# Performance work log

Hardware: AMD Instinct MI355X
Metric: run time of the kernel (lower is better)

Reference implementation:

```python
import jax, jax.numpy as jnp
import numpy as np
import math

EPS = 1e-06
C_CONST = 2.0 + EPS
CHUNK = 128


def _features(xc, omega, W_poly, quad_nodes):
    # xc: (B,H,t,D) -> poly:(B,H,t,P), prf:(R,B,H,t,M)
    xn = xc / jnp.clip(jnp.linalg.norm(xc, axis=-1, keepdims=True), 1e-12)  # F.normalize
    poly = jnp.einsum('bhtd,hdp->bhtp', xn, W_poly)
    proj = jnp.einsum('bhtd,rhdm->rbhtm', xn, omega)
    s = quad_nodes[:, None, None, None, None]
    sqrt2s = jnp.sqrt(2.0 * jnp.clip(s, 0.0))
    M = omega.shape[-1]
    prf = jnp.exp(jnp.clip(proj * sqrt2s - s, -20.0, 20.0)) / math.sqrt(M)
    return poly, prf


def setup_inputs() -> dict:
    key = jax.random.key(0)
    ks = jax.random.split(key, 6)
    B, T, E, H, D, M, R, P = 1, 1024, 512, 8, 64, 8, 1, 32
    x = jax.random.normal(ks[0], (B, T, E), jnp.float32)
    W_qkv = jax.random.normal(ks[1], (3 * E, E), jnp.float32) / math.sqrt(E)
    b_qkv = jnp.zeros((3 * E,), jnp.float32)
    W_out = jax.random.normal(ks[2], (E, E), jnp.float32) / math.sqrt(E)
    b_out = jnp.zeros((E,), jnp.float32)
    omega = jax.random.normal(ks[3], (R, H, D, M), jnp.float32)
    W_poly = jax.random.normal(ks[4], (H, D, P), jnp.float32) / math.sqrt(D)
    nodes, weights = np.polynomial.laguerre.laggauss(R)
    quad_nodes = jnp.asarray(nodes, jnp.float32) / C_CONST
    quad_weights = jnp.asarray(weights, jnp.float32) / C_CONST
    return {"x": x, "W_qkv": W_qkv, "b_qkv": b_qkv, "W_out": W_out, "b_out": b_out,
            "omega": omega, "W_poly": W_poly, "quad_nodes": quad_nodes, "quad_weights": quad_weights}


def reference(x, W_qkv, b_qkv, W_out, b_out, omega, W_poly, quad_nodes, quad_weights):
    B, T, E = x.shape
    R, H, D, M = omega.shape
    P = W_poly.shape[-1]
    qkv = x @ W_qkv.T + b_qkv
    q, k, v = jnp.split(qkv, 3, axis=-1)

    def to_chunks(a):
        # (B,T,E) -> (Nc,B,H,chunk,D)
        return a.reshape(B, T, H, D).transpose(0, 2, 1, 3).reshape(B, H, T // CHUNK, CHUNK, D).transpose(2, 0, 1, 3, 4)

    qc, kc, vc = map(to_chunks, (q, k, v))
    sqw = jnp.sqrt(jnp.clip(quad_weights, 0.0))[:, None, None, None, None]
    kv0 = jnp.zeros((R, B, H, P, M, D), jnp.float32)
    k0 = jnp.zeros((R, B, H, P, M), jnp.float32)

    def step(carry, inp):
        kv_state, k_state = carry
        qch, kch, vch = inp
        q_poly, q_prf = _features(qch, omega, W_poly, quad_nodes)
        k_poly, k_prf = _features(kch, omega, W_poly, quad_nodes)
        q_prf = q_prf * sqw
        k_prf = k_prf * sqw
        q_outer = jnp.einsum('bhtp,rbhtm->rbhtpm', q_poly, q_prf)
        k_outer = jnp.einsum('bhtp,rbhtm->rbhtpm', k_poly, k_prf)
        kv_prod = jnp.einsum('rbhtpm,bhtd->rbhtpmd', k_outer, vch)
        kv_cur = jnp.cumsum(kv_prod, axis=3) + kv_state[:, :, :, None]
        k_cur = jnp.cumsum(k_outer, axis=3) + k_state[:, :, :, None]
        ctx = jnp.einsum('rbhtpm,rbhtpmd->bhtd', q_outer, kv_cur)  # sums over r too
        den = jnp.einsum('rbhtpm,rbhtpm->bht', q_outer, k_cur)
        out = ctx / jnp.clip(den, 1e-06)[..., None]
        return (kv_cur[:, :, :, -1], k_cur[:, :, :, -1]), out

    _, outs = jax.lax.scan(step, (kv0, k0), (qc, kc, vc))  # (Nc,B,H,chunk,D)
    out = outs.transpose(1, 2, 0, 3, 4).reshape(B, H, T, D).transpose(0, 2, 1, 3).reshape(B, T, E)
    return out @ W_out.T + b_out
```

## Files before the change

kernel.cpp:

```cpp
#include <hip/hip_runtime.h>
#include <math.h>


__global__ __launch_bounds__(256) void gemm_bias_kernel(
    const float* __restrict__ A, const float* __restrict__ W,
    const float* __restrict__ bias, float* __restrict__ C,
    int M, int N, int K)
{
    __shared__ float a_t[16][68];
    __shared__ float w_t[16][68];
    const int tid = threadIdx.x;
    const int n0 = blockIdx.x * 64;
    const int m0 = blockIdx.y * 64;
    const int tx = tid & 15, ty = tid >> 4;
    const int lrow = tid >> 2;
    const int lk4  = (tid & 3) * 4;
    float acc[4][4];
#pragma unroll
    for (int i = 0; i < 4; ++i)
#pragma unroll
        for (int j = 0; j < 4; ++j) acc[i][j] = 0.f;

    for (int k0 = 0; k0 < K; k0 += 16) {
        float4 av = *(const float4*)&A[(m0 + lrow) * K + k0 + lk4];
        float4 wv = *(const float4*)&W[(n0 + lrow) * K + k0 + lk4];
        a_t[lk4 + 0][lrow] = av.x; a_t[lk4 + 1][lrow] = av.y;
        a_t[lk4 + 2][lrow] = av.z; a_t[lk4 + 3][lrow] = av.w;
        w_t[lk4 + 0][lrow] = wv.x; w_t[lk4 + 1][lrow] = wv.y;
        w_t[lk4 + 2][lrow] = wv.z; w_t[lk4 + 3][lrow] = wv.w;
        __syncthreads();
#pragma unroll
        for (int k = 0; k < 16; ++k) {
            float4 af = *(const float4*)&a_t[k][ty * 4];
            float4 wf = *(const float4*)&w_t[k][tx * 4];
            acc[0][0] += af.x * wf.x; acc[0][1] += af.x * wf.y;
            acc[0][2] += af.x * wf.z; acc[0][3] += af.x * wf.w;
            acc[1][0] += af.y * wf.x; acc[1][1] += af.y * wf.y;
            acc[1][2] += af.y * wf.z; acc[1][3] += af.y * wf.w;
            acc[2][0] += af.z * wf.x; acc[2][1] += af.z * wf.y;
            acc[2][2] += af.z * wf.z; acc[2][3] += af.z * wf.w;
            acc[3][0] += af.w * wf.x; acc[3][1] += af.w * wf.y;
            acc[3][2] += af.w * wf.z; acc[3][3] += af.w * wf.w;
        }
        __syncthreads();
    }
    float4 bv = *(const float4*)&bias[n0 + tx * 4];
#pragma unroll
    for (int i = 0; i < 4; ++i) {
        float4 o;
        o.x = acc[i][0] + bv.x; o.y = acc[i][1] + bv.y;
        o.z = acc[i][2] + bv.z; o.w = acc[i][3] + bv.w;
        *(float4*)&C[(m0 + ty * 4 + i) * N + n0 + tx * 4] = o;
    }
}

__global__ __launch_bounds__(256) void features_kernel(
    const float* __restrict__ qkv, const float* __restrict__ omega,
    const float* __restrict__ W_poly, const float* __restrict__ qn,
    const float* __restrict__ qw, float* __restrict__ phi_q,
    float* __restrict__ phi_k)
{
    __shared__ float xn[4][2][64];
    __shared__ float poly[4][2][32];
    __shared__ float prf[4][2][8];
    const int tid = threadIdx.x;
    const int w = tid >> 6;
    const int lane = tid & 63;
    const int item = blockIdx.x * 4 + w;
    const int h = item >> 10;
    const int t = item & 1023;

    float xq = qkv[t * 1536 + h * 64 + lane];
    float xk = qkv[t * 1536 + 512 + h * 64 + lane];
    float sq = xq * xq, sk = xk * xk;
#pragma unroll
    for (int o = 32; o; o >>= 1) { sq += __shfl_xor(sq, o); sk += __shfl_xor(sk, o); }
    float xnq = xq / fmaxf(sqrtf(sq), 1e-12f);
    float xnk = xk / fmaxf(sqrtf(sk), 1e-12f);
    xn[w][0][lane] = xnq;
    xn[w][1][lane] = xnk;
    __syncthreads();

    {
        const int which = lane >> 5;
        const int p = lane & 31;
        float pacc = 0.f;
#pragma unroll 8
        for (int d = 0; d < 64; ++d)
            pacc += xn[w][which][d] * W_poly[(h * 64 + d) * 32 + p];
        poly[w][which][p] = pacc;
    }
    if (lane < 16) {
        const int wh2 = lane >> 3, m = lane & 7;
        float pr = 0.f;
#pragma unroll 8
        for (int d = 0; d < 64; ++d)
            pr += xn[w][wh2][d] * omega[(h * 64 + d) * 8 + m];
        float s0 = qn[0];
        float sqrt2s = sqrtf(2.f * fmaxf(s0, 0.f));
        float sqw = sqrtf(fmaxf(qw[0], 0.f));
        float z = fminf(fmaxf(pr * sqrt2s - s0, -20.f), 20.f);
        prf[w][wh2][m] = expf(z) * 0.3535533905932738f * sqw;
    }
    __syncthreads();

    const int pp = lane >> 1;
    const int mb = (lane & 1) * 4;
    float qp = poly[w][0][pp], kp = poly[w][1][pp];
    float4 oq, ok;
    oq.x = qp * prf[w][0][mb + 0]; oq.y = qp * prf[w][0][mb + 1];
    oq.z = qp * prf[w][0][mb + 2]; oq.w = qp * prf[w][0][mb + 3];
    ok.x = kp * prf[w][1][mb + 0]; ok.y = kp * prf[w][1][mb + 1];
    ok.z = kp * prf[w][1][mb + 2]; ok.w = kp * prf[w][1][mb + 3];
    *(float4*)&phi_q[((h << 10) + t) * 256 + lane * 4] = oq;
    *(float4*)&phi_k[((h << 10) + t) * 256 + lane * 4] = ok;
}

__global__ __launch_bounds__(256) void chunksum_kernel(
    const float* __restrict__ phi_k, const float* __restrict__ qkv,
    float* __restrict__ S_chunk, float* __restrict__ z_chunk)
{
    __shared__ float pk[128][64];
    __shared__ float vv[128][64];
    const int tid = threadIdx.x;
    const int h  = blockIdx.x >> 5;
    const int c  = (blockIdx.x >> 2) & 7;
    const int fg = blockIdx.x & 3;
    const int f0 = fg * 64;

#pragma unroll
    for (int i = 0; i < 8; ++i) {
        int e4 = i * 256 + tid;
        int s = e4 >> 4;
        int f4 = (e4 & 15) * 4;
        *(float4*)&pk[s][f4] =
            *(const float4*)&phi_k[((h << 10) + c * 128 + s) * 256 + f0 + f4];
    }
#pragma unroll
    for (int i = 0; i < 8; ++i) {
        int e4 = i * 256 + tid;
        int s = e4 >> 4;
        int d4 = (e4 & 15) * 4;
        *(float4*)&vv[s][d4] =
            *(const float4*)&qkv[(c * 128 + s) * 1536 + 1024 + h * 64 + d4];
    }
    __syncthreads();

    const int tx = tid & 15;
    const int ty = tid >> 4;
    float acc[4][4];
#pragma unroll
    for (int i = 0; i < 4; ++i)
#pragma unroll
        for (int j = 0; j < 4; ++j) acc[i][j] = 0.f;

    for (int s = 0; s < 128; ++s) {
        float4 pv = *(const float4*)&pk[s][ty * 4];
        float4 v4 = *(const float4*)&vv[s][tx * 4];
        acc[0][0] += pv.x * v4.x; acc[0][1] += pv.x * v4.y;
        acc[0][2] += pv.x * v4.z; acc[0][3] += pv.x * v4.w;
        acc[1][0] += pv.y * v4.x; acc[1][1] += pv.y * v4.y;
        acc[1][2] += pv.y * v4.z; acc[1][3] += pv.y * v4.w;
        acc[2][0] += pv.z * v4.x; acc[2][1] += pv.z * v4.y;
        acc[2][2] += pv.z * v4.z; acc[2][3] += pv.z * v4.w;
        acc[3][0] += pv.w * v4.x; acc[3][1] += pv.w * v4.y;
        acc[3][2] += pv.w * v4.z; acc[3][3] += pv.w * v4.w;
    }

    if (tid < 64) {
        float zacc = 0.f;
        for (int s = 0; s < 128; ++s) zacc += pk[s][tid];
        z_chunk[(h * 8 + c) * 256 + f0 + tid] = zacc;
    }

#pragma unroll
    for (int i = 0; i < 4; ++i) {
        float4 o = make_float4(acc[i][0], acc[i][1], acc[i][2], acc[i][3]);
        *(float4*)&S_chunk[((h * 8 + c) * 256 + f0 + ty * 4 + i) * 64 + tx * 4] = o;
    }
}

__global__ __launch_bounds__(256) void scan_kernel(
    const float* __restrict__ S_chunk, const float* __restrict__ z_chunk,
    float* __restrict__ S_prev, float* __restrict__ z_prev)
{
    int gid = blockIdx.x * 256 + threadIdx.x;
    if (gid < 8 * 256 * 64) {
        int h = gid >> 14;
        int r = gid & 16383;
        float acc = 0.f;
#pragma unroll
        for (int c = 0; c < 8; ++c) {
            int idx = ((h * 8 + c) << 14) + r;
            S_prev[idx] = acc;
            acc += S_chunk[idx];
        }
    }
    if (gid < 2048) {
        int h = gid >> 8, f = gid & 255;
        float acc = 0.f;
#pragma unroll
        for (int c = 0; c < 8; ++c) {
            int idx = (h * 8 + c) * 256 + f;
            z_prev[idx] = acc;
            acc += z_chunk[idx];
        }
    }
}

__global__ __launch_bounds__(256) void attn_kernel(
    const float* __restrict__ phi_q, const float* __restrict__ phi_k,
    const float* __restrict__ qkv, const float* __restrict__ S_prev,
    const float* __restrict__ z_prev, float* __restrict__ attn)
{
    __shared__ float v_lds[128 * 64];
    __shared__ float A_lds[32 * 132];
    __shared__ float phq_t[32][36];
    __shared__ float phk_t[32][132];
    __shared__ float Sst[32][64];
    __shared__ float z_lds[256];
    __shared__ float den_lds[32];
    const int tid = threadIdx.x;
    const int h = blockIdx.x >> 3, c = blockIdx.x & 7;
    const int tb = blockIdx.y * 32;

#pragma unroll
    for (int i = 0; i < 8; ++i) {
        int e4 = i * 256 + tid;
        int s = e4 >> 4;
        int d4 = (e4 & 15) * 4;
        *(float4*)&v_lds[s * 64 + d4] =
            *(const float4*)&qkv[(c * 128 + s) * 1536 + 1024 + h * 64 + d4];
    }
    z_lds[tid] = z_prev[(h * 8 + c) * 256 + tid];

    const int tt = tid >> 5, ss = tid & 31;
    const int d = tid & 63, tg = tid >> 6;
    float acc[4][4];
    float acc2[8];
    float den_acc = 0.f;
#pragma unroll
    for (int i = 0; i < 4; ++i)
#pragma unroll
        for (int j = 0; j < 4; ++j) acc[i][j] = 0.f;
#pragma unroll
    for (int i = 0; i < 8; ++i) acc2[i] = 0.f;

    for (int ft = 0; ft < 8; ++ft) {
        const int f0 = ft * 32;
#pragma unroll
        for (int i = 0; i < 4; ++i) {
            int e = i * 256 + tid;
            int t_ = e >> 5, f = e & 31;
            phq_t[f][t_] = phi_q[((h << 10) + c * 128 + tb + t_) * 256 + f0 + f];
        }
#pragma unroll
        for (int i = 0; i < 16; ++i) {
            int e = i * 256 + tid;
            int s_ = e >> 5, f = e & 31;
            phk_t[f][s_] = phi_k[((h << 10) + c * 128 + s_) * 256 + f0 + f];
        }
#pragma unroll
        for (int i = 0; i < 8; ++i) {
            int e = i * 256 + tid;
            int f = e >> 6, dd = e & 63;
            Sst[f][dd] = S_prev[((h * 8 + c) * 256 + f0 + f) * 64 + dd];
        }
        __syncthreads();
#pragma unroll 4
        for (int f = 0; f < 32; ++f) {
            float4 av = *(const float4*)&phq_t[f][tt * 4];
            float4 bv = *(const float4*)&phk_t[f][ss * 4];
            acc[0][0] += av.x * bv.x; acc[0][1] += av.x * bv.y;
            acc[0][2] += av.x * bv.z; acc[0][3] += av.x * bv.w;
            acc[1][0] += av.y * bv.x; acc[1][1] += av.y * bv.y;
            acc[1][2] += av.y * bv.z; acc[1][3] += av.y * bv.w;
            acc[2][0] += av.z * bv.x; acc[2][1] += av.z * bv.y;
            acc[2][2] += av.z * bv.z; acc[2][3] += av.z * bv.w;
            acc[3][0] += av.w * bv.x; acc[3][1] += av.w * bv.y;
            acc[3][2] += av.w * bv.z; acc[3][3] += av.w * bv.w;
            float sval = Sst[f][d];
            float4 a0 = *(const float4*)&phq_t[f][tg * 8];
            float4 a1 = *(const float4*)&phq_t[f][tg * 8 + 4];
            acc2[0] += a0.x * sval; acc2[1] += a0.y * sval;
            acc2[2] += a0.z * sval; acc2[3] += a0.w * sval;
            acc2[4] += a1.x * sval; acc2[5] += a1.y * sval;
            acc2[6] += a1.z * sval; acc2[7] += a1.w * sval;
        }
        if (tid < 32) {
#pragma unroll
            for (int f = 0; f < 32; ++f)
                den_acc += phq_t[f][tid] * z_lds[f0 + f];
        }
        __syncthreads();
    }
#pragma unroll
    for (int i = 0; i < 4; ++i) {
        float4 o = make_float4(acc[i][0], acc[i][1], acc[i][2], acc[i][3]);
        *(float4*)&A_lds[(tt * 4 + i) * 132 + ss * 4] = o;
    }
    if (tid < 32) den_lds[tid] = den_acc;
    __syncthreads();

#pragma unroll
    for (int i = 0; i < 8; ++i) {
        int tl = tg * 8 + i;
        int tcr = tb + tl;
        float ctx = acc2[i];
        float den = den_lds[tl];
        for (int s = 0; s <= tcr; ++s) {
            float a = A_lds[tl * 132 + s];
            ctx += a * v_lds[s * 64 + d];
            den += a;
        }
        attn[(c * 128 + tcr) * 512 + h * 64 + d] = ctx / fmaxf(den, 1e-6f);
    }
}

extern "C" void kernel_launch(void* const* d_in, const int* in_sizes, int n_in,
                              void* d_out, int out_size, void* d_ws, size_t ws_size,
                              hipStream_t stream)
{
    const float* x      = (const float*)d_in[0];
    const float* W_qkv  = (const float*)d_in[1];
    const float* b_qkv  = (const float*)d_in[2];
    const float* W_out  = (const float*)d_in[3];
    const float* b_out  = (const float*)d_in[4];
    const float* omega  = (const float*)d_in[5];
    const float* W_poly = (const float*)d_in[6];
    const float* qn     = (const float*)d_in[7];
    const float* qw     = (const float*)d_in[8];
    float* out = (float*)d_out;

    float* ws    = (float*)d_ws;
    float* qkv   = ws;
    float* phi_q = qkv + 1572864;
    float* phi_k = phi_q + 2097152;
    float* S_c   = phi_k + 2097152;
    float* z_c   = S_c + 1048576;
    float* S_p   = z_c + 16384;
    float* z_p   = S_p + 1048576;
    float* attn  = z_p + 16384;

    gemm_bias_kernel<<<dim3(24, 16), 256, 0, stream>>>(x, W_qkv, b_qkv, qkv, 1024, 1536, 512);
    features_kernel<<<2048, 256, 0, stream>>>(qkv, omega, W_poly, qn, qw, phi_q, phi_k);
    chunksum_kernel<<<256, 256, 0, stream>>>(phi_k, qkv, S_c, z_c);
    scan_kernel<<<512, 256, 0, stream>>>(S_c, z_c, S_p, z_p);
    attn_kernel<<<dim3(64, 4), 256, 0, stream>>>(phi_q, phi_k, qkv, S_p, z_p, attn);
    gemm_bias_kernel<<<dim3(8, 16), 256, 0, stream>>>(attn, W_out, b_out, out, 1024, 512, 512);
}
```

Before: 198.2 us.

## Split attn kernel into 512-thread warp-specialized halves and skip non-causal key tiles

The attention kernel now launches 512 threads per block. Half compute the intra-chunk q·k scores, the other half compute the inter-chunk q·S context and the denominator, with results passed through a new shared buffer. It also loads only the keys and values up to the causal limit for each query tile and skips score tiles beyond it. The intent is more parallelism per block and less wasted load and FMA work, at the cost of extra shared memory and an extra LDS round trip.

```diff
diff --git a/kernel.cpp b/kernel.cpp
--- a/kernel.cpp
+++ b/kernel.cpp
@@ -208,7 +208,7 @@
     }
 }
 
-__global__ __launch_bounds__(256) void attn_kernel(
+__global__ __launch_bounds__(512, 2) void attn_kernel(
     const float* __restrict__ phi_q, const float* __restrict__ phi_k,
     const float* __restrict__ qkv, const float* __restrict__ S_prev,
     const float* __restrict__ z_prev, float* __restrict__ attn)
@@ -218,24 +218,27 @@
     __shared__ float phq_t[32][36];
     __shared__ float phk_t[32][132];
     __shared__ float Sst[32][64];
+    __shared__ float ctx_lds[32][68];
     __shared__ float z_lds[256];
     __shared__ float den_lds[32];
     const int tid = threadIdx.x;
     const int h = blockIdx.x >> 3, c = blockIdx.x & 7;
-    const int tb = blockIdx.y * 32;
-
-#pragma unroll
-    for (int i = 0; i < 8; ++i) {
-        int e4 = i * 256 + tid;
+    const int q = blockIdx.y;
+    const int tb = q * 32;
+    const int SMAX = tb + 32;
+
+    for (int e4 = tid; e4 < SMAX * 16; e4 += 512) {
         int s = e4 >> 4;
         int d4 = (e4 & 15) * 4;
         *(float4*)&v_lds[s * 64 + d4] =
             *(const float4*)&qkv[(c * 128 + s) * 1536 + 1024 + h * 64 + d4];
     }
-    z_lds[tid] = z_prev[(h * 8 + c) * 256 + tid];
+    if (tid < 256) z_lds[tid] = z_prev[(h * 8 + c) * 256 + tid];
 
     const int tt = tid >> 5, ss = tid & 31;
-    const int d = tid & 63, tg = tid >> 6;
+    const bool ssActive = (ss * 4) < SMAX;
+    const int u = tid & 255;
+    const int d = u & 63, tg = u >> 6;
     float acc[4][4];
     float acc2[8];
     float den_acc = 0.f;
@@ -249,71 +252,89 @@
     for (int ft = 0; ft < 8; ++ft) {
         const int f0 = ft * 32;
 #pragma unroll
-        for (int i = 0; i < 4; ++i) {
-            int e = i * 256 + tid;
+        for (int k = 0; k < 2; ++k) {
+            int e = k * 512 + tid;
             int t_ = e >> 5, f = e & 31;
             phq_t[f][t_] = phi_q[((h << 10) + c * 128 + tb + t_) * 256 + f0 + f];
         }
-#pragma unroll
-        for (int i = 0; i < 16; ++i) {
-            int e = i * 256 + tid;
+        for (int e = tid; e < 32 * SMAX; e += 512) {
             int s_ = e >> 5, f = e & 31;
             phk_t[f][s_] = phi_k[((h << 10) + c * 128 + s_) * 256 + f0 + f];
         }
 #pragma unroll
-        for (int i = 0; i < 8; ++i) {
-            int e = i * 256 + tid;
+        for (int k = 0; k < 4; ++k) {
+            int e = k * 512 + tid;
             int f = e >> 6, dd = e & 63;
             Sst[f][dd] = S_prev[((h * 8 + c) * 256 + f0 + f) * 64 + dd];
         }
         __syncthreads();
+
+        if (tid < 256) {
+            if (ssActive) {
 #pragma unroll 4
-        for (int f = 0; f < 32; ++f) {
-            float4 av = *(const float4*)&phq_t[f][tt * 4];
-            float4 bv = *(const float4*)&phk_t[f][ss * 4];
-            acc[0][0] += av.x * bv.x; acc[0][1] += av.x * bv.y;
-            acc[0][2] += av.x * bv.z; acc[0][3] += av.x * bv.w;
-            acc[1][0] += av.y * bv.x; acc[1][1] += av.y * bv.y;
-            acc[1][2] += av.y * bv.z; acc[1][3] += av.y * bv.w;
-            acc[2][0] += av.z * bv.x; acc[2][1] += av.z * bv.y;
-            acc[2][2] += av.z * bv.z; acc[2][3] += av.z * bv.w;
-            acc[3][0] += av.w * bv.x; acc[3][1] += av.w * bv.y;
-            acc[3][2] += av.w * bv.z; acc[3][3] += av.w * bv.w;
-            float sval = Sst[f][d];
-            float4 a0 = *(const float4*)&phq_t[f][tg * 8];
-            float4 a1 = *(const float4*)&phq_t[f][tg * 8 + 4];
-            acc2[0] += a0.x * sval; acc2[1] += a0.y * sval;
-            acc2[2] += a0.z * sval; acc2[3] += a0.w * sval;
-            acc2[4] += a1.x * sval; acc2[5] += a1.y * sval;
-            acc2[6] += a1.z * sval; acc2[7] += a1.w * sval;
-        }
-        if (tid < 32) {
-#pragma unroll
-            for (int f = 0; f < 32; ++f)
-                den_acc += phq_t[f][tid] * z_lds[f0 + f];
+                for (int f = 0; f < 32; ++f) {
+                    float4 av = *(const float4*)&phq_t[f][tt * 4];
+                    float4 bv = *(const float4*)&phk_t[f][ss * 4];
+                    acc[0][0] += av.x * bv.x; acc[0][1] += av.x * bv.y;
+                    acc[0][2] += av.x * bv.z; acc[0][3] += av.x * bv.w;
+                    acc[1][0] += av.y * bv.x; acc[1][1] += av.y * bv.y;
+                    acc[1][2] += av.y * bv.z; acc[1][3] += av.y * bv.w;
+                    acc[2][0] += av.z * bv.x; acc[2][1] += av.z * bv.y;
+                    acc[2][2] += av.z * bv.z; acc[2][3] += av.z * bv.w;
+                    acc[3][0] += av.w * bv.x; acc[3][1] += av.w * bv.y;
+                    acc[3][2] += av.w * bv.z; acc[3][3] += av.w * bv.w;
+                }
+            }
+        } else {
+#pragma unroll 4
+            for (int f = 0; f < 32; ++f) {
+                float sval = Sst[f][d];
+                float4 a0 = *(const float4*)&phq_t[f][tg * 8];
+                float4 a1 = *(const float4*)&phq_t[f][tg * 8 + 4];
+                acc2[0] += a0.x * sval; acc2[1] += a0.y * sval;
+                acc2[2] += a0.z * sval; acc2[3] += a0.w * sval;
+                acc2[4] += a1.x * sval; acc2[5] += a1.y * sval;
+                acc2[6] += a1.z * sval; acc2[7] += a1.w * sval;
+            }
+            if (u < 32) {
+#pragma unroll
+                for (int f = 0; f < 32; ++f)
+                    den_acc += phq_t[f][u] * z_lds[f0 + f];
+            }
         }
         __syncthreads();
     }
+
+    if (tid < 256) {
+        if (ssActive) {
+#pragma unroll
+            for (int i = 0; i < 4; ++i) {
+                float4 o = make_float4(acc[i][0], acc[i][1], acc[i][2], acc[i][3]);
+                *(float4*)&A_lds[(tt * 4 + i) * 132 + ss * 4] = o;
+            }
+        }
+    } else {
+#pragma unroll
+        for (int i = 0; i < 8; ++i)
+            ctx_lds[tg * 8 + i][d] = acc2[i];
+        if (u < 32) den_lds[u] = den_acc;
+    }
+    __syncthreads();
+
+    const int dd = tid & 63;
+    const int rg = tid >> 6;
 #pragma unroll
     for (int i = 0; i < 4; ++i) {
-        float4 o = make_float4(acc[i][0], acc[i][1], acc[i][2], acc[i][3]);
-        *(float4*)&A_lds[(tt * 4 + i) * 132 + ss * 4] = o;
-    }
-    if (tid < 32) den_lds[tid] = den_acc;
-    __syncthreads();
-
-#pragma unroll
-    for (int i = 0; i < 8; ++i) {
-        int tl = tg * 8 + i;
+        int tl = rg * 4 + i;
         int tcr = tb + tl;
-        float ctx = acc2[i];
+        float ctx = ctx_lds[tl][dd];
         float den = den_lds[tl];
         for (int s = 0; s <= tcr; ++s) {
             float a = A_lds[tl * 132 + s];
-            ctx += a * v_lds[s * 64 + d];
+            ctx += a * v_lds[s * 64 + dd];
             den += a;
         }
-        attn[(c * 128 + tcr) * 512 + h * 64 + d] = ctx / fmaxf(den, 1e-6f);
+        attn[(c * 128 + tcr) * 512 + h * 64 + dd] = ctx / fmaxf(den, 1e-6f);
     }
 }
 
@@ -346,6 +367,6 @@
     features_kernel<<<2048, 256, 0, stream>>>(qkv, omega, W_poly, qn, qw, phi_q, phi_k);
     chunksum_kernel<<<256, 256, 0, stream>>>(phi_k, qkv, S_c, z_c);
     scan_kernel<<<512, 256, 0, stream>>>(S_c, z_c, S_p, z_p);
-    attn_kernel<<<dim3(64, 4), 256, 0, stream>>>(phi_q, phi_k, qkv, S_p, z_p, attn);
+    attn_kernel<<<dim3(64, 4), 512, 0, stream>>>(phi_q, phi_k, qkv, S_p, z_p, attn);
     gemm_bias_kernel<<<dim3(8, 16), 256, 0, stream>>>(attn, W_out, b_out, out, 1024, 512, 512);
 }
```

Measured after the change: 198.5 us. Within noise of the previous version (+0.1%).
